# Kernel tuning notes

Hardware: AMD Instinct MI355X
Metric: run time of the kernel (lower is better)

Reference implementation:

```python
import jax, jax.numpy as jnp
import numpy as np

DIM = 512
BATCH = 64
SRC_L = 2048


def setup_inputs() -> dict:
    key = jax.random.key(0)
    ks = jax.random.split(key, 7)
    s = 1.0 / np.sqrt(DIM)
    return {
        "query": jax.random.normal(ks[0], (BATCH, DIM), dtype=jnp.float32),
        "ref": jax.random.normal(ks[1], (SRC_L, BATCH, DIM), dtype=jnp.float32),
        # nn.Linear(dim, dim)
        "Wq": jax.random.uniform(ks[2], (DIM, DIM), jnp.float32, -s, s),
        "bq": jax.random.uniform(ks[3], (DIM,), jnp.float32, -s, s),
        # nn.Conv1d(dim, dim, 1, 1) -> weight [out, in, 1] squeezed to [out, in]
        "Wr": jax.random.uniform(ks[4], (DIM, DIM), jnp.float32, -s, s),
        "br": jax.random.uniform(ks[5], (DIM,), jnp.float32, -s, s),
        # self.v ~ U(-1/sqrt(dim), 1/sqrt(dim))
        "v": jax.random.uniform(ks[6], (DIM,), jnpp := jnp.float32, -s, s),
    }


def reference(query, ref, Wq, bq, Wr, br, v):
    # ref: [L, B, D] -> [B, D, L]
    ref_bdl = jnp.transpose(ref, (1, 2, 0))
    # q = Linear(query): [B, D] -> broadcast as [B, D, 1]
    q = query @ Wq.T + bq  # [B, D]
    # e = 1x1 Conv1d over ref: pointwise GEMM along channel dim
    e = jnp.einsum("oi,bil->bol", Wr, ref_bdl) + br[None, :, None]  # [B, D, L]
    # u = v . tanh(q + e) reduced over D (fused broadcast-add-tanh-reduce)
    u = jnp.einsum("d,bdl->bl", v, jnp.tanh(q[:, :, None] + e))  # [B, L]
    logits = u  # use_tanh=False
    return (e, logits)
```

## Files before the change

kernel.cpp:

```cpp
#include <hip/hip_runtime.h>

#define DIM 512
#define B_  64
#define L_  2048

typedef unsigned short u16;
typedef float f32x4 __attribute__((ext_vector_type(4)));
typedef short s16x8 __attribute__((ext_vector_type(8)));
typedef short s16x4 __attribute__((ext_vector_type(4)));

__device__ __forceinline__ u16 f2bf(float f) {
  union { float f; unsigned u; } x{f};
  unsigned r = x.u + 0x7FFFu + ((x.u >> 16) & 1u);
  return (u16)(r >> 16);
}

__device__ __forceinline__ float tanh_fast(float x) {
  float e2 = __expf(2.0f * x);
  return 1.0f - 2.0f / (e2 + 1.0f);
}

__global__ __launch_bounds__(256) void prep_kernel(
    const float* __restrict__ query, const float* __restrict__ Wq,
    const float* __restrict__ bq, const float* __restrict__ Wr,
    float* __restrict__ q_out, u16* __restrict__ Wrb) {
  const int blk = blockIdx.x;
  const int tid = threadIdx.x;
  if (blk < 64) {
    __shared__ float qs[DIM];
    for (int i = tid; i < DIM; i += 256) qs[i] = query[blk * DIM + i];
    __syncthreads();
    for (int o = tid; o < DIM; o += 256) {
      const float* w = Wq + o * DIM;
      float acc = 0.f;
      for (int k = 0; k < DIM; k += 4) {
        f32x4 a = *(const f32x4*)&qs[k];
        f32x4 b = *(const f32x4*)&w[k];
        acc += a.x * b.x + a.y * b.y + a.z * b.z + a.w * b.w;
      }
      q_out[blk * DIM + o] = acc + bq[o];
    }
  } else {
    const int c = blk - 64;
    const int base = c * 4096 + tid * 16;
#pragma unroll
    for (int i = 0; i < 4; ++i) {
      f32x4 a = *(const f32x4*)&Wr[base + i * 4];
      s16x4 o4;
      o4.x = (short)f2bf(a.x); o4.y = (short)f2bf(a.y);
      o4.z = (short)f2bf(a.z); o4.w = (short)f2bf(a.w);
      *(s16x4*)&Wrb[base + i * 4] = o4;
    }
  }
}

__global__ __launch_bounds__(512, 1) void attn_main(
    const float* __restrict__ ref, const u16* __restrict__ Wrb,
    const float* __restrict__ q, const float* __restrict__ br,
    const float* __restrict__ v, float* __restrict__ e_out,
    float* __restrict__ logits) {
  __shared__ u16 As[2][4][128][8];
  __shared__ u16 Bs[128][520];
  __shared__ float u_lds[2][128];

  const int lt = blockIdx.x, b = blockIdx.y;
  const int l0 = lt * 128;
  const int tid = threadIdx.x;
  const int lane = tid & 63;
  const int w = tid >> 6;
  const int wr = w >> 2, wc = w & 3;
  const int rr = lane & 15, kg = lane >> 4;

  const int skc = tid >> 7;
  const int soP = tid & 127;
  const int soL = soP ^ (skc << 1);

  s16x8 a0 = *(const s16x8*)&Wrb[(size_t)soL * DIM + skc * 8];
#pragma unroll
  for (int g = 0; g < 4; ++g) {
    f32x4 r[8];
#pragma unroll
    for (int i = 0; i < 8; ++i) {
      int flat = g * 4096 + i * 512 + tid;
      int row = flat >> 7, c = flat & 127;
      r[i] = *(const f32x4*)&ref[(size_t)(l0 + row) * (B_ * DIM) + (size_t)b * DIM + c * 4];
    }
#pragma unroll
    for (int i = 0; i < 8; ++i) {
      int flat = g * 4096 + i * 512 + tid;
      int row = flat >> 7, c = flat & 127;
      s16x4 o4;
      o4.x = (short)f2bf(r[i].x); o4.y = (short)f2bf(r[i].y);
      o4.z = (short)f2bf(r[i].z); o4.w = (short)f2bf(r[i].w);
      *(s16x4*)&Bs[row][c * 4] = o4;
    }
  }
  *(s16x8*)&As[0][skc][soP][0] = a0;
  __syncthreads();

  f32x4 accT[2][4];
#pragma unroll
  for (int fn = 0; fn < 2; ++fn)
#pragma unroll
    for (int fm = 0; fm < 4; ++fm) accT[fn][fm] = (f32x4){0.f, 0.f, 0.f, 0.f};

  for (int s = 0; s < 64; ++s) {
    const int cur = s & 1, t = s & 15, ot = s >> 4;
    s16x8 anx;
    if (s < 63) {
      const int sn = s + 1, otn = sn >> 4, tn = sn & 15;
      anx = *(const s16x8*)&Wrb[(size_t)((otn << 7) + soL) * DIM + tn * 32 + skc * 8];
    }
    s16x8 af[4], bf[2];
#pragma unroll
    for (int fm = 0; fm < 4; ++fm) {
      int row = wr * 64 + fm * 16 + rr;
      af[fm] = *(const s16x8*)&As[cur][kg][row ^ (kg << 1)][0];
    }
#pragma unroll
    for (int fn = 0; fn < 2; ++fn)
      bf[fn] = *(const s16x8*)&Bs[wc * 32 + fn * 16 + rr][t * 32 + kg * 8];
#pragma unroll
    for (int fn = 0; fn < 2; ++fn)
#pragma unroll
      for (int fm = 0; fm < 4; ++fm)
        accT[fn][fm] = __builtin_amdgcn_mfma_f32_16x16x32_bf16(bf[fn], af[fm], accT[fn][fm], 0, 0, 0);
    if (s < 63) *(s16x8*)&As[cur ^ 1][skc][soP][0] = anx;
    __syncthreads();

    if (t == 15) {
      const int ob = (ot << 7) + wr * 64;
      float bb[4], vv[4], qq[4];
#pragma unroll
      for (int fm = 0; fm < 4; ++fm) {
        int o = ob + fm * 16 + rr;
        bb[fm] = br[o]; vv[fm] = v[o]; qq[fm] = q[b * DIM + o] + bb[fm];
      }
#pragma unroll
      for (int fn = 0; fn < 2; ++fn) {
        f32x4 us = (f32x4){0.f, 0.f, 0.f, 0.f};
        const int lb = l0 + wc * 32 + fn * 16 + kg * 4;
#pragma unroll
        for (int fm = 0; fm < 4; ++fm) {
          int o = ob + fm * 16 + rr;
          f32x4 a = accT[fn][fm];
          f32x4 ev = a + bb[fm];
          __builtin_nontemporal_store(ev, (f32x4*)&e_out[((size_t)(b * DIM + o)) * L_ + lb]);
          f32x4 th;
          th.x = tanh_fast(a.x + qq[fm]);
          th.y = tanh_fast(a.y + qq[fm]);
          th.z = tanh_fast(a.z + qq[fm]);
          th.w = tanh_fast(a.w + qq[fm]);
          us += vv[fm] * th;
          accT[fn][fm] = (f32x4){0.f, 0.f, 0.f, 0.f};
        }
#pragma unroll
        for (int msk = 1; msk <= 8; msk <<= 1) {
          us.x += __shfl_xor(us.x, msk);
          us.y += __shfl_xor(us.y, msk);
          us.z += __shfl_xor(us.z, msk);
          us.w += __shfl_xor(us.w, msk);
        }
        if (rr == 0) {
          float* up = &u_lds[wr][wc * 32 + fn * 16 + kg * 4];
          if (ot == 0) {
            *(f32x4*)up = us;
          } else {
            f32x4 old = *(f32x4*)up;
            *(f32x4*)up = old + us;
          }
        }
      }
    }
  }
  __syncthreads();
  if (tid < 128)
    logits[(size_t)b * L_ + l0 + tid] = u_lds[0][tid] + u_lds[1][tid];
}

extern "C" void kernel_launch(void* const* d_in, const int* in_sizes, int n_in,
                              void* d_out, int out_size, void* d_ws, size_t ws_size,
                              hipStream_t stream) {
  const float* query = (const float*)d_in[0];
  const float* ref   = (const float*)d_in[1];
  const float* Wq    = (const float*)d_in[2];
  const float* bq    = (const float*)d_in[3];
  const float* Wr    = (const float*)d_in[4];
  const float* br    = (const float*)d_in[5];
  const float* v     = (const float*)d_in[6];

  float* e_out  = (float*)d_out;
  float* logits = e_out + (size_t)B_ * DIM * L_;

  char* ws = (char*)d_ws;
  u16*   Wrb = (u16*)ws;
  float* q   = (float*)(ws + 524288);

  prep_kernel<<<128, 256, 0, stream>>>(query, Wq, bq, Wr, q, Wrb);
  attn_main<<<dim3(16, 64), 512, 0, stream>>>(ref, Wrb, q, br, v, e_out, logits);
}
```

Measured before the change: 262.4 us.

## Drop LDS staging; load MFMA fragments directly from global with K-tiled weight layout

The main kernel no longer stages ref and weights through shared memory. Each wave loads its ref fragments straight from global memory, converts them to bf16 with packed-convert instructions, and prefetches the next K slice while the current one runs through MFMA. Weights are pre-laid out in K-tile-major order so fragment loads are contiguous, and each wave now owns a 128x64 output tile held in registers. This removes the per-step barriers and LDS traffic, and launch bounds allow two blocks per CU. The cost is much higher register pressure from 32 accumulators and redundant global loads of ref and weights across waves, served from cache.

```diff
diff --git a/kernel.cpp b/kernel.cpp
--- a/kernel.cpp
+++ b/kernel.cpp
@@ -20,10 +20,19 @@
   return 1.0f - 2.0f / (e2 + 1.0f);
 }
 
+__device__ __forceinline__ s16x8 cvt8(f32x4 a, f32x4 b) {
+  union { s16x8 h; unsigned u[4]; } r;
+  asm("v_cvt_pk_bf16_f32 %0, %1, %2" : "=v"(r.u[0]) : "v"(a.x), "v"(a.y));
+  asm("v_cvt_pk_bf16_f32 %0, %1, %2" : "=v"(r.u[1]) : "v"(a.z), "v"(a.w));
+  asm("v_cvt_pk_bf16_f32 %0, %1, %2" : "=v"(r.u[2]) : "v"(b.x), "v"(b.y));
+  asm("v_cvt_pk_bf16_f32 %0, %1, %2" : "=v"(r.u[3]) : "v"(b.z), "v"(b.w));
+  return r.h;
+}
+
 __global__ __launch_bounds__(256) void prep_kernel(
     const float* __restrict__ query, const float* __restrict__ Wq,
     const float* __restrict__ bq, const float* __restrict__ Wr,
-    float* __restrict__ q_out, u16* __restrict__ Wrb) {
+    float* __restrict__ q_out, u16* __restrict__ Wrbt) {
   const int blk = blockIdx.x;
   const int tid = threadIdx.x;
   if (blk < 64) {
@@ -42,140 +51,118 @@
     }
   } else {
     const int c = blk - 64;
-    const int base = c * 4096 + tid * 16;
+    const int flat = c * 4096 + tid * 16;
+    const int o = flat >> 9, k0 = flat & 511;
+    const int t = k0 >> 5, kk = k0 & 31;
+    u16* dst = Wrbt + t * 16384 + o * 32 + kk;
 #pragma unroll
     for (int i = 0; i < 4; ++i) {
-      f32x4 a = *(const f32x4*)&Wr[base + i * 4];
+      f32x4 a = *(const f32x4*)&Wr[flat + i * 4];
       s16x4 o4;
       o4.x = (short)f2bf(a.x); o4.y = (short)f2bf(a.y);
       o4.z = (short)f2bf(a.z); o4.w = (short)f2bf(a.w);
-      *(s16x4*)&Wrb[base + i * 4] = o4;
+      *(s16x4*)&dst[i * 4] = o4;
     }
   }
 }
 
-__global__ __launch_bounds__(512, 1) void attn_main(
-    const float* __restrict__ ref, const u16* __restrict__ Wrb,
+__global__ __launch_bounds__(512, 2) void attn_main(
+    const float* __restrict__ ref, const u16* __restrict__ Wrbt,
     const float* __restrict__ q, const float* __restrict__ br,
     const float* __restrict__ v, float* __restrict__ e_out,
     float* __restrict__ logits) {
-  __shared__ u16 As[2][4][128][8];
-  __shared__ u16 Bs[128][520];
-  __shared__ float u_lds[2][128];
+  __shared__ float u_lds[4][128];
 
   const int lt = blockIdx.x, b = blockIdx.y;
   const int l0 = lt * 128;
-  const int tid = threadIdx.x;
-  const int lane = tid & 63;
-  const int w = tid >> 6;
-  const int wr = w >> 2, wc = w & 3;
+  const int tid = threadIdx.x, lane = tid & 63, w = tid >> 6;
+  const int ow = w >> 1, lw = w & 1;
   const int rr = lane & 15, kg = lane >> 4;
 
-  const int skc = tid >> 7;
-  const int soP = tid & 127;
-  const int soL = soP ^ (skc << 1);
+  const float* refp[4];
+#pragma unroll
+  for (int fn = 0; fn < 4; ++fn)
+    refp[fn] = ref + (size_t)(l0 + lw * 64 + fn * 16 + rr) * (B_ * DIM)
+             + (size_t)b * DIM + kg * 8;
+  const u16* ap = Wrbt + (ow * 128 + rr) * 32 + kg * 8;
 
-  s16x8 a0 = *(const s16x8*)&Wrb[(size_t)soL * DIM + skc * 8];
+  f32x4 rn[4][2];
 #pragma unroll
-  for (int g = 0; g < 4; ++g) {
-    f32x4 r[8];
+  for (int fn = 0; fn < 4; ++fn) {
+    rn[fn][0] = *(const f32x4*)(refp[fn]);
+    rn[fn][1] = *(const f32x4*)(refp[fn] + 4);
+  }
+
+  f32x4 acc[8][4];
 #pragma unroll
-    for (int i = 0; i < 8; ++i) {
-      int flat = g * 4096 + i * 512 + tid;
-      int row = flat >> 7, c = flat & 127;
-      r[i] = *(const f32x4*)&ref[(size_t)(l0 + row) * (B_ * DIM) + (size_t)b * DIM + c * 4];
+  for (int fm = 0; fm < 8; ++fm)
+#pragma unroll
+    for (int fn = 0; fn < 4; ++fn) acc[fm][fn] = (f32x4){0.f, 0.f, 0.f, 0.f};
+
+  for (int t = 0; t < 16; ++t) {
+    s16x8 af[8];
+#pragma unroll
+    for (int fm = 0; fm < 8; ++fm)
+      af[fm] = *(const s16x8*)(ap + t * 16384 + fm * 512);
+    s16x8 bf[4];
+#pragma unroll
+    for (int fn = 0; fn < 4; ++fn) bf[fn] = cvt8(rn[fn][0], rn[fn][1]);
+    if (t < 15) {
+#pragma unroll
+      for (int fn = 0; fn < 4; ++fn) {
+        rn[fn][0] = *(const f32x4*)(refp[fn] + (t + 1) * 32);
+        rn[fn][1] = *(const f32x4*)(refp[fn] + (t + 1) * 32 + 4);
+      }
     }
 #pragma unroll
-    for (int i = 0; i < 8; ++i) {
-      int flat = g * 4096 + i * 512 + tid;
-      int row = flat >> 7, c = flat & 127;
-      s16x4 o4;
-      o4.x = (short)f2bf(r[i].x); o4.y = (short)f2bf(r[i].y);
-      o4.z = (short)f2bf(r[i].z); o4.w = (short)f2bf(r[i].w);
-      *(s16x4*)&Bs[row][c * 4] = o4;
+    for (int fm = 0; fm < 8; ++fm)
+#pragma unroll
+      for (int fn = 0; fn < 4; ++fn)
+        acc[fm][fn] = __builtin_amdgcn_mfma_f32_16x16x32_bf16(bf[fn], af[fm], acc[fm][fn], 0, 0, 0);
+  }
+
+  const int ob = ow * 128;
+  f32x4 usA[4];
+#pragma unroll
+  for (int fn = 0; fn < 4; ++fn) usA[fn] = (f32x4){0.f, 0.f, 0.f, 0.f};
+#pragma unroll
+  for (int fm = 0; fm < 8; ++fm) {
+    const int o = ob + fm * 16 + rr;
+    const float brv = br[o];
+    const float qv = q[b * DIM + o] + brv;
+    const float vv = v[o];
+    const size_t erow = ((size_t)(b * DIM + o)) * L_;
+#pragma unroll
+    for (int fn = 0; fn < 4; ++fn) {
+      const int lb = l0 + lw * 64 + fn * 16 + kg * 4;
+      f32x4 a = acc[fm][fn];
+      f32x4 ev = a + brv;
+      __builtin_nontemporal_store(ev, (f32x4*)&e_out[erow + lb]);
+      f32x4 th;
+      th.x = tanh_fast(a.x + qv);
+      th.y = tanh_fast(a.y + qv);
+      th.z = tanh_fast(a.z + qv);
+      th.w = tanh_fast(a.w + qv);
+      usA[fn] += vv * th;
     }
   }
-  *(s16x8*)&As[0][skc][soP][0] = a0;
-  __syncthreads();
-
-  f32x4 accT[2][4];
 #pragma unroll
-  for (int fn = 0; fn < 2; ++fn)
+  for (int fn = 0; fn < 4; ++fn) {
+    f32x4 us = usA[fn];
 #pragma unroll
-    for (int fm = 0; fm < 4; ++fm) accT[fn][fm] = (f32x4){0.f, 0.f, 0.f, 0.f};
-
-  for (int s = 0; s < 64; ++s) {
-    const int cur = s & 1, t = s & 15, ot = s >> 4;
-    s16x8 anx;
-    if (s < 63) {
-      const int sn = s + 1, otn = sn >> 4, tn = sn & 15;
-      anx = *(const s16x8*)&Wrb[(size_t)((otn << 7) + soL) * DIM + tn * 32 + skc * 8];
+    for (int msk = 1; msk <= 8; msk <<= 1) {
+      us.x += __shfl_xor(us.x, msk);
+      us.y += __shfl_xor(us.y, msk);
+      us.z += __shfl_xor(us.z, msk);
+      us.w += __shfl_xor(us.w, msk);
     }
-    s16x8 af[4], bf[2];
-#pragma unroll
-    for (int fm = 0; fm < 4; ++fm) {
-      int row = wr * 64 + fm * 16 + rr;
-      af[fm] = *(const s16x8*)&As[cur][kg][row ^ (kg << 1)][0];
-    }
-#pragma unroll
-    for (int fn = 0; fn < 2; ++fn)
-      bf[fn] = *(const s16x8*)&Bs[wc * 32 + fn * 16 + rr][t * 32 + kg * 8];
-#pragma unroll
-    for (int fn = 0; fn < 2; ++fn)
-#pragma unroll
-      for (int fm = 0; fm < 4; ++fm)
-        accT[fn][fm] = __builtin_amdgcn_mfma_f32_16x16x32_bf16(bf[fn], af[fm], accT[fn][fm], 0, 0, 0);
-    if (s < 63) *(s16x8*)&As[cur ^ 1][skc][soP][0] = anx;
-    __syncthreads();
-
-    if (t == 15) {
-      const int ob = (ot << 7) + wr * 64;
-      float bb[4], vv[4], qq[4];
-#pragma unroll
-      for (int fm = 0; fm < 4; ++fm) {
-        int o = ob + fm * 16 + rr;
-        bb[fm] = br[o]; vv[fm] = v[o]; qq[fm] = q[b * DIM + o] + bb[fm];
-      }
-#pragma unroll
-      for (int fn = 0; fn < 2; ++fn) {
-        f32x4 us = (f32x4){0.f, 0.f, 0.f, 0.f};
-        const int lb = l0 + wc * 32 + fn * 16 + kg * 4;
-#pragma unroll
-        for (int fm = 0; fm < 4; ++fm) {
-          int o = ob + fm * 16 + rr;
-          f32x4 a = accT[fn][fm];
-          f32x4 ev = a + bb[fm];
-          __builtin_nontemporal_store(ev, (f32x4*)&e_out[((size_t)(b * DIM + o)) * L_ + lb]);
-          f32x4 th;
-          th.x = tanh_fast(a.x + qq[fm]);
-          th.y = tanh_fast(a.y + qq[fm]);
-          th.z = tanh_fast(a.z + qq[fm]);
-          th.w = tanh_fast(a.w + qq[fm]);
-          us += vv[fm] * th;
-          accT[fn][fm] = (f32x4){0.f, 0.f, 0.f, 0.f};
-        }
-#pragma unroll
-        for (int msk = 1; msk <= 8; msk <<= 1) {
-          us.x += __shfl_xor(us.x, msk);
-          us.y += __shfl_xor(us.y, msk);
-          us.z += __shfl_xor(us.z, msk);
-          us.w += __shfl_xor(us.w, msk);
-        }
-        if (rr == 0) {
-          float* up = &u_lds[wr][wc * 32 + fn * 16 + kg * 4];
-          if (ot == 0) {
-            *(f32x4*)up = us;
-          } else {
-            f32x4 old = *(f32x4*)up;
-            *(f32x4*)up = old + us;
-          }
-        }
-      }
-    }
+    if (rr == 0)
+      *(f32x4*)&u_lds[ow][lw * 64 + fn * 16 + kg * 4] = us;
   }
   __syncthreads();
   if (tid < 128)
-    logits[(size_t)b * L_ + l0 + tid] = u_lds[0][tid] + u_lds[1][tid];
+    logits[(size_t)b * L_ + l0 + tid] =
+        u_lds[0][tid] + u_lds[1][tid] + u_lds[2][tid] + u_lds[3][tid];
 }
 
 extern "C" void kernel_launch(void* const* d_in, const int* in_sizes, int n_in,
@@ -193,9 +180,9 @@
   float* logits = e_out + (size_t)B_ * DIM * L_;
 
   char* ws = (char*)d_ws;
-  u16*   Wrb = (u16*)ws;
-  float* q   = (float*)(ws + 524288);
+  u16*   Wrbt = (u16*)ws;
+  float* q    = (float*)(ws + 524288);
 
-  prep_kernel<<<128, 256, 0, stream>>>(query, Wq, bq, Wr, q, Wrb);
-  attn_main<<<dim3(16, 64), 512, 0, stream>>>(ref, Wrb, q, br, v, e_out, logits);
+  prep_kernel<<<128, 256, 0, stream>>>(query, Wq, bq, Wr, q, Wrbt);
+  attn_main<<<dim3(16, 64), 512, 0, stream>>>(ref, Wrbt, q, br, v, e_out, logits);
 }
```

Result: slower. 308.7 us (+17.7%).
